# Optimization experiments

Measured on AMD Instinct MI355X. Metric: run time of the kernel, lower is better.

The kernel has to match this reference:

```python
import jax, jax.numpy as jnp
import numpy as np

EMB = 512
HEADS = 8


def setup_inputs() -> dict:
    key = jax.random.key(0)
    ks = jax.random.split(key, 5)
    B, N, E = 4, 2048, EMB
    x = jax.random.normal(ks[0], (B, N, E), dtype=jnp.float32)
    # Linear weights stored [in, out] so y = x @ W + b (matches torch x @ W.T + b with W.T)
    W_qkv = jax.random.normal(ks[1], (E, 3 * E), dtype=jnp.float32) * (E ** -0.5)
    b_qkv = jax.random.normal(ks[2], (3 * E,), dtype=jnp.float32) * 0.02
    W_proj = jax.random.normal(ks[3], (E, E), dtype=jnp.float32) * (E ** -0.5)
    b_proj = jax.random.normal(ks[4], (E,), dtype=jnp.float32) * 0.02
    return {"x": x, "W_qkv": W_qkv, "b_qkv": b_qkv, "W_proj": W_proj, "b_proj": b_proj}


def reference(x, W_qkv, b_qkv, W_proj, b_proj):
    B, N, E = x.shape
    H = HEADS
    D = E // H
    qkv = x @ W_qkv + b_qkv                      # [B, N, 3E]
    # einops 'b n (h d qkv) -> qkv b h n d': last dim splits as (h, d, 3) -> q/k/v interleaved
    qkv = qkv.reshape(B, N, H, D, 3)
    q = jnp.transpose(qkv[..., 0], (0, 2, 1, 3))  # [B, H, N, D]
    k = jnp.transpose(qkv[..., 1], (0, 2, 1, 3))
    v = jnp.transpose(qkv[..., 2], (0, 2, 1, 3))
    scale = jnp.asarray(E, x.dtype) ** 0.5        # divides by sqrt(emb_size), as in source
    energies = jnp.einsum('bhqd,bhkd->bhqk', q, k) / scale
    attention = jax.nn.softmax(energies, axis=-1)
    out = jnp.einsum('bhqk,bhkd->bhqd', attention, v)
    out = jnp.transpose(out, (0, 2, 1, 3)).reshape(B, N, E)
    return out @ W_proj + b_proj
```

## Files before the change

kernel.cpp:

```cpp
#include <hip/hip_runtime.h>
#include <hip/hip_bf16.h>

typedef __hip_bfloat16 bf16;
typedef __attribute__((ext_vector_type(8))) short short8;
typedef __attribute__((ext_vector_type(4))) float f32x4;
typedef __attribute__((ext_vector_type(16))) float f32x16;

static constexpr float QSCALE = 1.4426950408889634f / 22.627416997969522f;

__device__ __forceinline__ void gload_lds16(const void* g, void* l) {
  __builtin_amdgcn_global_load_lds((const __attribute__((address_space(1))) unsigned*)(g),
                                   (__attribute__((address_space(3))) unsigned*)(l), 16, 0, 0);
}

__device__ __forceinline__ unsigned cvtpk(float a, float b) {
  unsigned r;
  asm("v_cvt_pk_bf16_f32 %0, %1, %2" : "=v"(r) : "v"(a), "v"(b));
  return r;
}

__global__ __launch_bounds__(256) void cvt_x_kernel(const float* __restrict__ x,
                                                    bf16* __restrict__ xb, int n8) {
  for (int i = blockIdx.x * 256 + threadIdx.x; i < n8; i += gridDim.x * 256) {
    const float4* src = (const float4*)(x) + (size_t)i * 2;
    float4 a = src[0], b = src[1];
    union { short8 v; unsigned u[4]; } o;
    o.u[0] = cvtpk(a.x, a.y);
    o.u[1] = cvtpk(a.z, a.w);
    o.u[2] = cvtpk(b.x, b.y);
    o.u[3] = cvtpk(b.z, b.w);
    *(short8*)(xb + (size_t)i * 8) = o.v;
  }
}

__global__ __launch_bounds__(256) void transpose_cvt(const float* __restrict__ W,
                                                     bf16* __restrict__ Wt,
                                                     int Nout, int permute) {
  __shared__ float tile[64][65];
  const int j0 = blockIdx.x * 64, k0 = blockIdx.y * 64;
  const int tx = threadIdx.x & 63, ty = threadIdx.x >> 6;
  for (int r = ty; r < 64; r += 4)
    tile[r][tx] = W[(size_t)(k0 + r) * Nout + j0 + tx];
  __syncthreads();
  for (int r = ty; r < 64; r += 4) {
    int j = j0 + r;
    int jp = j;
    if (permute) {
      int h = j / 192, rr = j % 192, d = rr / 3, s = rr % 3;
      jp = s * 512 + h * 64 + d;
    }
    Wt[(size_t)jp * 512 + k0 + tx] = __float2bfloat16(tile[tx][r]);
  }
}

template <int MODE>
__global__ __launch_bounds__(256) void gemm_bt(const bf16* __restrict__ A,
                                               const bf16* __restrict__ Bt,
                                               const float* __restrict__ bias,
                                               bf16* __restrict__ Qb, bf16* __restrict__ Kb,
                                               bf16* __restrict__ Vt,
                                               float* __restrict__ Cout) {
  __shared__ short Alds[128 * 32];
  __shared__ short Blds[128 * 32];
  const int t = threadIdx.x;
  const int w = t >> 6;
  const int wr = w >> 1, wc = w & 1;
  const int lr = t & 15;
  const int lq = (t >> 4) & 3;
  const int bm = blockIdx.x, bn = blockIdx.y;

  f32x4 acc[4][4];
#pragma unroll
  for (int m = 0; m < 4; ++m)
#pragma unroll
    for (int n = 0; n < 4; ++n)
#pragma unroll
      for (int j = 0; j < 4; ++j) acc[m][n][j] = 0.f;

  for (int kt = 0; kt < 16; ++kt) {
#pragma unroll
    for (int i = 0; i < 2; ++i) {
      const int c = i * 256 + t;
      gload_lds16(A + (size_t)(bm * 128 + (c >> 2)) * 512 + kt * 32 + (c & 3) * 8,
                  &Alds[(i * 256 + w * 64) * 8]);
      gload_lds16(Bt + (size_t)(bn * 128 + (c >> 2)) * 512 + kt * 32 + (c & 3) * 8,
                  &Blds[(i * 256 + w * 64) * 8]);
    }
    __syncthreads();
    short8 af[4], bfr[4];
#pragma unroll
    for (int m = 0; m < 4; ++m)
      af[m] = *(const short8*)&Alds[(wr * 64 + m * 16 + lr) * 32 + lq * 8];
#pragma unroll
    for (int n = 0; n < 4; ++n)
      bfr[n] = *(const short8*)&Blds[(wc * 64 + n * 16 + lr) * 32 + lq * 8];
#pragma unroll
    for (int m = 0; m < 4; ++m)
#pragma unroll
      for (int n = 0; n < 4; ++n)
        acc[m][n] = __builtin_amdgcn_mfma_f32_16x16x32_bf16(af[m], bfr[n], acc[m][n], 0, 0, 0);
    __syncthreads();
  }

#pragma unroll
  for (int m = 0; m < 4; ++m) {
#pragma unroll
    for (int n = 0; n < 4; ++n) {
      const int col = bn * 128 + wc * 64 + n * 16 + lr;
#pragma unroll
      for (int j = 0; j < 4; ++j) {
        const int row = bm * 128 + wr * 64 + m * 16 + lq * 4 + j;
        float v = acc[m][n][j];
        if (MODE == 0) {
          const int s = col >> 9, h = (col >> 6) & 7, d = col & 63;
          v += bias[h * 192 + d * 3 + s];
          const int hd = col & 511;
          if (s == 0)
            Qb[(size_t)row * 512 + hd] = __float2bfloat16(v * QSCALE);
          else if (s == 1)
            Kb[(size_t)row * 512 + hd] = __float2bfloat16(v);
          else
            Vt[((size_t)((row >> 11) * 8 + h) * 64 + d) * 2048 + (row & 2047)] =
                __float2bfloat16(v);
        } else {
          v += bias[col];
          Cout[(size_t)row * 512 + col] = v;
        }
      }
    }
  }
}

__global__ __launch_bounds__(128) void attn_fwd(const bf16* __restrict__ Q,
                                                const bf16* __restrict__ K,
                                                const bf16* __restrict__ Vt,
                                                bf16* __restrict__ O) {
  __shared__ short Klds[2][64 * 64];
  __shared__ short Vlds[2][64 * 64];
  const int t = threadIdx.x;
  const int w = t >> 6;
  const int l = t & 63;
  const int lo = l & 31;
  const int hi = l >> 5;
  const int bid = blockIdx.x;
  const int bh = bid & 31, qt = bid >> 5;
  const int b = bh >> 3, h = bh & 7;
  const int qgA = qt * 128 + w * 64 + lo;

  const bf16* Kb = K + (size_t)b * 2048 * 512 + h * 64;
  const bf16* Vb = Vt + (size_t)bh * 64 * 2048;

  const bf16* qptrA = Q + ((size_t)b * 2048 + qgA) * 512 + h * 64 + hi * 8;
  short8 qfA[4], qfB[4];
#pragma unroll
  for (int kk = 0; kk < 4; ++kk) {
    qfA[kk] = *(const short8*)(qptrA + kk * 16);
    qfB[kk] = *(const short8*)(qptrA + 32 * 512 + kk * 16);
  }

  f32x16 zv;
#pragma unroll
  for (int r = 0; r < 16; ++r) zv[r] = 0.f;

  f32x16 accA0, accA1, accB0, accB1;
#pragma unroll
  for (int r = 0; r < 16; ++r) { accA0[r] = 0.f; accA1[r] = 0.f; accB0[r] = 0.f; accB1[r] = 0.f; }
  float lsA = 0.f, lsB = 0.f;

#define STAGE(BUF, KV0)                                                              \
  do {                                                                               \
    _Pragma("unroll") for (int i = 0; i < 4; ++i) {                                  \
      const int c = i * 128 + t, r = c >> 3, g = (c & 7) ^ (r & 7);                  \
      gload_lds16(Kb + (size_t)((KV0) + r) * 512 + g * 8,                            \
                  &Klds[BUF][(i * 128 + w * 64) * 8]);                               \
    }                                                                                \
    _Pragma("unroll") for (int i = 0; i < 4; ++i) {                                  \
      const int c = i * 128 + t, r = c >> 3, g = (c & 7) ^ (r & 7);                  \
      gload_lds16(Vb + (size_t)r * 2048 + (KV0) + g * 8,                             \
                  &Vlds[BUF][(i * 128 + w * 64) * 8]);                               \
    }                                                                                \
  } while (0)

  STAGE(0, 0);
  __syncthreads();

#pragma unroll 2
  for (int it = 0; it < 32; ++it) {
    const int buf = it & 1;
    if (it + 1 < 32) STAGE(buf ^ 1, (it + 1) * 64);

    const char* kl = (const char*)&Klds[buf][0];
    const char* vl = (const char*)&Vlds[buf][0];

#pragma unroll
    for (int sh = 0; sh < 2; ++sh) {
      short8 kf[4];
#pragma unroll
      for (int kk = 0; kk < 4; ++kk)
        kf[kk] = *(const short8*)(kl + ((sh * 32 + lo) << 7) +
                                  ((((kk << 1) | hi) ^ (lo & 7)) << 4));

      f32x16 sA, sB;
      __builtin_amdgcn_s_setprio(1);
#pragma unroll
      for (int kk = 0; kk < 4; ++kk) {
        sA = __builtin_amdgcn_mfma_f32_32x32x16_bf16(kf[kk], qfA[kk], kk ? sA : zv, 0, 0, 0);
        sB = __builtin_amdgcn_mfma_f32_32x32x16_bf16(kf[kk], qfB[kk], kk ? sB : zv, 0, 0, 0);
      }
      __builtin_amdgcn_s_setprio(0);

      short8 vf[2][2];
#pragma unroll
      for (int dt = 0; dt < 2; ++dt)
#pragma unroll
        for (int j = 0; j < 2; ++j)
          vf[dt][j] = *(const short8*)(vl + ((dt * 32 + lo) << 7) +
                                       (((((sh * 2 + j) << 1) | hi) ^ (lo & 7)) << 4));

      float tA = 0.f, tB = 0.f;
#pragma unroll
      for (int r = 0; r < 16; ++r) { sA[r] = __builtin_amdgcn_exp2f(sA[r]); tA += sA[r]; }
#pragma unroll
      for (int r = 0; r < 16; ++r) { sB[r] = __builtin_amdgcn_exp2f(sB[r]); tB += sB[r]; }
      lsA += tA;
      lsB += tB;

      short8 pbA[2], pbB[2];
#pragma unroll
      for (int g = 0; g < 2; ++g) {
        {
          unsigned a0 = cvtpk(sA[8 * g + 0], sA[8 * g + 1]);
          unsigned a1 = cvtpk(sA[8 * g + 2], sA[8 * g + 3]);
          unsigned b0 = cvtpk(sA[8 * g + 4], sA[8 * g + 5]);
          unsigned b1 = cvtpk(sA[8 * g + 6], sA[8 * g + 7]);
          asm("v_permlane32_swap_b32 %0, %1" : "+v"(a0), "+v"(b0));
          asm("v_permlane32_swap_b32 %0, %1" : "+v"(a1), "+v"(b1));
          union { unsigned u[4]; short8 v; } pu;
          pu.u[0] = a0; pu.u[1] = a1; pu.u[2] = b0; pu.u[3] = b1;
          pbA[g] = pu.v;
        }
        {
          unsigned a0 = cvtpk(sB[8 * g + 0], sB[8 * g + 1]);
          unsigned a1 = cvtpk(sB[8 * g + 2], sB[8 * g + 3]);
          unsigned b0 = cvtpk(sB[8 * g + 4], sB[8 * g + 5]);
          unsigned b1 = cvtpk(sB[8 * g + 6], sB[8 * g + 7]);
          asm("v_permlane32_swap_b32 %0, %1" : "+v"(a0), "+v"(b0));
          asm("v_permlane32_swap_b32 %0, %1" : "+v"(a1), "+v"(b1));
          union { unsigned u[4]; short8 v; } pu;
          pu.u[0] = a0; pu.u[1] = a1; pu.u[2] = b0; pu.u[3] = b1;
          pbB[g] = pu.v;
        }
      }

      __builtin_amdgcn_s_setprio(1);
#pragma unroll
      for (int j = 0; j < 2; ++j) {
        accA0 = __builtin_amdgcn_mfma_f32_32x32x16_bf16(vf[0][j], pbA[j], accA0, 0, 0, 0);
        accA1 = __builtin_amdgcn_mfma_f32_32x32x16_bf16(vf[1][j], pbA[j], accA1, 0, 0, 0);
        accB0 = __builtin_amdgcn_mfma_f32_32x32x16_bf16(vf[0][j], pbB[j], accB0, 0, 0, 0);
        accB1 = __builtin_amdgcn_mfma_f32_32x32x16_bf16(vf[1][j], pbB[j], accB1, 0, 0, 0);
      }
      __builtin_amdgcn_s_setprio(0);
    }

    __syncthreads();
  }
#undef STAGE

  lsA += __shfl_xor(lsA, 32);
  lsB += __shfl_xor(lsB, 32);
  const float rlA = 1.0f / lsA;
  const float rlB = 1.0f / lsB;
  bf16* opA = O + ((size_t)b * 2048 + qgA) * 512 + h * 64;
  bf16* opB = opA + 32 * 512;
#pragma unroll
  for (int r = 0; r < 16; ++r) {
    const int d = (r & 3) + 8 * (r >> 2) + 4 * hi;
    opA[d] = __float2bfloat16(accA0[r] * rlA);
    opA[32 + d] = __float2bfloat16(accA1[r] * rlA);
    opB[d] = __float2bfloat16(accB0[r] * rlB);
    opB[32 + d] = __float2bfloat16(accB1[r] * rlB);
  }
}

extern "C" void kernel_launch(void* const* d_in, const int* in_sizes, int n_in,
                              void* d_out, int out_size, void* d_ws, size_t ws_size,
                              hipStream_t stream) {
  const float* x = (const float*)d_in[0];
  const float* Wqkv = (const float*)d_in[1];
  const float* bqkv = (const float*)d_in[2];
  const float* Wproj = (const float*)d_in[3];
  const float* bproj = (const float*)d_in[4];
  float* out = (float*)d_out;

  char* ws = (char*)d_ws;
  bf16* xb = (bf16*)ws;
  bf16* Wqkvt = xb + (size_t)8192 * 512;
  bf16* Wprojt = Wqkvt + (size_t)1536 * 512;
  bf16* Qb = Wprojt + (size_t)512 * 512;
  bf16* Kb = Qb + (size_t)8192 * 512;
  bf16* Vt = Kb + (size_t)8192 * 512;
  bf16* Ob = xb;

  cvt_x_kernel<<<2048, 256, 0, stream>>>(x, xb, 8192 * 512 / 8);
  transpose_cvt<<<dim3(24, 8), 256, 0, stream>>>(Wqkv, Wqkvt, 1536, 1);
  transpose_cvt<<<dim3(8, 8), 256, 0, stream>>>(Wproj, Wprojt, 512, 0);
  gemm_bt<0><<<dim3(64, 12), 256, 0, stream>>>(xb, Wqkvt, bqkv, Qb, Kb, Vt, nullptr);
  attn_fwd<<<512, 128, 0, stream>>>(Qb, Kb, Vt, Ob);
  gemm_bt<1><<<dim3(64, 4), 256, 0, stream>>>(Ob, Wprojt, bproj, nullptr, nullptr, nullptr, out);
}
```

Baseline: 106.9 us.

## Split KV range across wave pairs in attention and merge partials via LDS

Doubles attention block size to four waves, with each wave pair processing half of the key/value sequence for the same query rows. Both halves are staged into doubled LDS buffers, and the loop runs half as many iterations. At the end, one half writes its accumulators and row sums to LDS and the other adds them before normalizing and storing. This raises wave-level parallelism and shortens per-wave serial loop length, at the cost of doubled LDS footprint and an extra merge step with a barrier.

Measured after the change: 111.4 us. +4.3%, slower.

```diff
diff --git a/kernel.cpp b/kernel.cpp
--- a/kernel.cpp
+++ b/kernel.cpp
@@ -131,24 +131,27 @@
   }
 }
 
-__global__ __launch_bounds__(128) void attn_fwd(const bf16* __restrict__ Q,
+__global__ __launch_bounds__(256) void attn_fwd(const bf16* __restrict__ Q,
                                                 const bf16* __restrict__ K,
                                                 const bf16* __restrict__ Vt,
                                                 bf16* __restrict__ O) {
-  __shared__ short Klds[2][64 * 64];
-  __shared__ short Vlds[2][64 * 64];
+  __shared__ short Klds[2][2][64 * 64];
+  __shared__ short Vlds[2][2][64 * 64];
   const int t = threadIdx.x;
   const int w = t >> 6;
+  const int half = w & 1;
+  const int pair = w >> 1;
   const int l = t & 63;
   const int lo = l & 31;
   const int hi = l >> 5;
   const int bid = blockIdx.x;
   const int bh = bid & 31, qt = bid >> 5;
   const int b = bh >> 3, h = bh & 7;
-  const int qgA = qt * 128 + w * 64 + lo;
+  const int qgA = qt * 128 + pair * 64 + lo;
 
   const bf16* Kb = K + (size_t)b * 2048 * 512 + h * 64;
   const bf16* Vb = Vt + (size_t)bh * 64 * 2048;
+  const int kb0 = half * 1024;
 
   const bf16* qptrA = Q + ((size_t)b * 2048 + qgA) * 512 + h * 64 + hi * 8;
   short8 qfA[4], qfB[4];
@@ -167,30 +170,32 @@
   for (int r = 0; r < 16; ++r) { accA0[r] = 0.f; accA1[r] = 0.f; accB0[r] = 0.f; accB1[r] = 0.f; }
   float lsA = 0.f, lsB = 0.f;
 
-#define STAGE(BUF, KV0)                                                              \
-  do {                                                                               \
-    _Pragma("unroll") for (int i = 0; i < 4; ++i) {                                  \
-      const int c = i * 128 + t, r = c >> 3, g = (c & 7) ^ (r & 7);                  \
-      gload_lds16(Kb + (size_t)((KV0) + r) * 512 + g * 8,                            \
-                  &Klds[BUF][(i * 128 + w * 64) * 8]);                               \
-    }                                                                                \
-    _Pragma("unroll") for (int i = 0; i < 4; ++i) {                                  \
-      const int c = i * 128 + t, r = c >> 3, g = (c & 7) ^ (r & 7);                  \
-      gload_lds16(Vb + (size_t)r * 2048 + (KV0) + g * 8,                             \
-                  &Vlds[BUF][(i * 128 + w * 64) * 8]);                               \
-    }                                                                                \
+#define STAGE(BUF, KV0)                                                               \
+  do {                                                                                \
+    _Pragma("unroll") for (int hf = 0; hf < 2; ++hf) {                                \
+      _Pragma("unroll") for (int i = 0; i < 2; ++i) {                                 \
+        const int c = i * 256 + t, r = c >> 3, g = (c & 7) ^ (r & 7);                 \
+        gload_lds16(Kb + (size_t)(hf * 1024 + (KV0) + r) * 512 + g * 8,               \
+                    &Klds[BUF][hf][(i * 256 + w * 64) * 8]);                          \
+      }                                                                               \
+      _Pragma("unroll") for (int i = 0; i < 2; ++i) {                                 \
+        const int c = i * 256 + t, r = c >> 3, g = (c & 7) ^ (r & 7);                 \
+        gload_lds16(Vb + (size_t)r * 2048 + hf * 1024 + (KV0) + g * 8,                \
+                    &Vlds[BUF][hf][(i * 256 + w * 64) * 8]);                          \
+      }                                                                               \
+    }                                                                                 \
   } while (0)
 
   STAGE(0, 0);
   __syncthreads();
 
 #pragma unroll 2
-  for (int it = 0; it < 32; ++it) {
+  for (int it = 0; it < 16; ++it) {
     const int buf = it & 1;
-    if (it + 1 < 32) STAGE(buf ^ 1, (it + 1) * 64);
-
-    const char* kl = (const char*)&Klds[buf][0];
-    const char* vl = (const char*)&Vlds[buf][0];
+    if (it + 1 < 16) STAGE(buf ^ 1, (it + 1) * 64);
+
+    const char* kl = (const char*)&Klds[buf][half][0];
+    const char* vl = (const char*)&Vlds[buf][half][0];
 
 #pragma unroll
     for (int sh = 0; sh < 2; ++sh) {
@@ -269,17 +274,45 @@
 
   lsA += __shfl_xor(lsA, 32);
   lsB += __shfl_xor(lsB, 32);
-  const float rlA = 1.0f / lsA;
-  const float rlB = 1.0f / lsB;
-  bf16* opA = O + ((size_t)b * 2048 + qgA) * 512 + h * 64;
-  bf16* opB = opA + 32 * 512;
-#pragma unroll
-  for (int r = 0; r < 16; ++r) {
-    const int d = (r & 3) + 8 * (r >> 2) + 4 * hi;
-    opA[d] = __float2bfloat16(accA0[r] * rlA);
-    opA[32 + d] = __float2bfloat16(accA1[r] * rlA);
-    opB[d] = __float2bfloat16(accB0[r] * rlB);
-    opB[32 + d] = __float2bfloat16(accB1[r] * rlB);
+
+  float* mrg = (float*)&Klds[0][0][0];
+  float* dnm = (float*)&Vlds[0][0][0];
+  if (half) {
+    float* base = mrg + pair * 4096;
+#pragma unroll
+    for (int r = 0; r < 16; ++r) {
+      base[l * 64 + ((r + l) & 63)] = accA0[r];
+      base[l * 64 + ((16 + r + l) & 63)] = accA1[r];
+      base[l * 64 + ((32 + r + l) & 63)] = accB0[r];
+      base[l * 64 + ((48 + r + l) & 63)] = accB1[r];
+    }
+    dnm[pair * 128 + l * 2] = lsA;
+    dnm[pair * 128 + l * 2 + 1] = lsB;
+  }
+  __syncthreads();
+  if (!half) {
+    float* base = mrg + pair * 4096;
+#pragma unroll
+    for (int r = 0; r < 16; ++r) {
+      accA0[r] += base[l * 64 + ((r + l) & 63)];
+      accA1[r] += base[l * 64 + ((16 + r + l) & 63)];
+      accB0[r] += base[l * 64 + ((32 + r + l) & 63)];
+      accB1[r] += base[l * 64 + ((48 + r + l) & 63)];
+    }
+    lsA += dnm[pair * 128 + l * 2];
+    lsB += dnm[pair * 128 + l * 2 + 1];
+    const float rlA = 1.0f / lsA;
+    const float rlB = 1.0f / lsB;
+    bf16* opA = O + ((size_t)b * 2048 + qgA) * 512 + h * 64;
+    bf16* opB = opA + 32 * 512;
+#pragma unroll
+    for (int r = 0; r < 16; ++r) {
+      const int d = (r & 3) + 8 * (r >> 2) + 4 * hi;
+      opA[d] = __float2bfloat16(accA0[r] * rlA);
+      opA[32 + d] = __float2bfloat16(accA1[r] * rlA);
+      opB[d] = __float2bfloat16(accB0[r] * rlB);
+      opB[32 + d] = __float2bfloat16(accB1[r] * rlB);
+    }
   }
 }
 
@@ -306,6 +339,6 @@
   transpose_cvt<<<dim3(24, 8), 256, 0, stream>>>(Wqkv, Wqkvt, 1536, 1);
   transpose_cvt<<<dim3(8, 8), 256, 0, stream>>>(Wproj, Wprojt, 512, 0);
   gemm_bt<0><<<dim3(64, 12), 256, 0, stream>>>(xb, Wqkvt, bqkv, Qb, Kb, Vt, nullptr);
-  attn_fwd<<<512, 128, 0, stream>>>(Qb, Kb, Vt, Ob);
+  attn_fwd<<<512, 256, 0, stream>>>(Qb, Kb, Vt, Ob);
   gemm_bt<1><<<dim3(64, 4), 256, 0, stream>>>(Ob, Wprojt, bproj, nullptr, nullptr, nullptr, out);
 }
```

## Compute softmax row sums via MFMA with ones and issue both QK halves upfront

Applied to the files above, without the earlier changes.

Restructures the attention inner loop so both 32-key halves of QK^T are computed before the exp/PV stages, which lets MFMA work overlap the exp and pack VALU work. Row sums are now accumulated with extra MFMAs against a ones vector instead of VALU adds and a cross-lane shuffle. Launch bounds now request at least one block per CU, which lets the compiler allocate more registers. The cost is 50% more PV-stage MFMAs, higher register pressure from the extra f32x16 accumulators, and row sums built from bf16-rounded probabilities.

After: 106.1 us. About the same (-0.7%).

```diff
diff --git a/kernel.cpp b/kernel.cpp
--- a/kernel.cpp
+++ b/kernel.cpp
@@ -17,6 +17,21 @@
   unsigned r;
   asm("v_cvt_pk_bf16_f32 %0, %1, %2" : "=v"(r) : "v"(a), "v"(b));
   return r;
+}
+
+__device__ __forceinline__ void packP(const f32x16& s, short8* pb) {
+#pragma unroll
+  for (int g = 0; g < 2; ++g) {
+    unsigned a0 = cvtpk(s[8 * g + 0], s[8 * g + 1]);
+    unsigned a1 = cvtpk(s[8 * g + 2], s[8 * g + 3]);
+    unsigned b0 = cvtpk(s[8 * g + 4], s[8 * g + 5]);
+    unsigned b1 = cvtpk(s[8 * g + 6], s[8 * g + 7]);
+    asm("v_permlane32_swap_b32 %0, %1" : "+v"(a0), "+v"(b0));
+    asm("v_permlane32_swap_b32 %0, %1" : "+v"(a1), "+v"(b1));
+    union { unsigned u[4]; short8 v; } pu;
+    pu.u[0] = a0; pu.u[1] = a1; pu.u[2] = b0; pu.u[3] = b1;
+    pb[g] = pu.v;
+  }
 }
 
 __global__ __launch_bounds__(256) void cvt_x_kernel(const float* __restrict__ x,
@@ -131,10 +146,10 @@
   }
 }
 
-__global__ __launch_bounds__(128) void attn_fwd(const bf16* __restrict__ Q,
-                                                const bf16* __restrict__ K,
-                                                const bf16* __restrict__ Vt,
-                                                bf16* __restrict__ O) {
+__global__ __launch_bounds__(128, 1) void attn_fwd(const bf16* __restrict__ Q,
+                                                   const bf16* __restrict__ K,
+                                                   const bf16* __restrict__ Vt,
+                                                   bf16* __restrict__ O) {
   __shared__ short Klds[2][64 * 64];
   __shared__ short Vlds[2][64 * 64];
   const int t = threadIdx.x;
@@ -158,14 +173,21 @@
     qfB[kk] = *(const short8*)(qptrA + 32 * 512 + kk * 16);
   }
 
+  union { unsigned u[4]; short8 v; } ones;
+#pragma unroll
+  for (int j = 0; j < 4; ++j) ones.u[j] = 0x3F803F80u;
+
   f32x16 zv;
 #pragma unroll
   for (int r = 0; r < 16; ++r) zv[r] = 0.f;
 
   f32x16 accA0, accA1, accB0, accB1;
-#pragma unroll
-  for (int r = 0; r < 16; ++r) { accA0[r] = 0.f; accA1[r] = 0.f; accB0[r] = 0.f; accB1[r] = 0.f; }
-  float lsA = 0.f, lsB = 0.f;
+  f32x16 ssumA, ssumB;
+#pragma unroll
+  for (int r = 0; r < 16; ++r) {
+    accA0[r] = 0.f; accA1[r] = 0.f; accB0[r] = 0.f; accB1[r] = 0.f;
+    ssumA[r] = 0.f; ssumB[r] = 0.f;
+  }
 
 #define STAGE(BUF, KV0)                                                              \
   do {                                                                               \
@@ -192,85 +214,89 @@
     const char* kl = (const char*)&Klds[buf][0];
     const char* vl = (const char*)&Vlds[buf][0];
 
-#pragma unroll
-    for (int sh = 0; sh < 2; ++sh) {
-      short8 kf[4];
-#pragma unroll
-      for (int kk = 0; kk < 4; ++kk)
-        kf[kk] = *(const short8*)(kl + ((sh * 32 + lo) << 7) +
-                                  ((((kk << 1) | hi) ^ (lo & 7)) << 4));
-
-      f32x16 sA, sB;
-      __builtin_amdgcn_s_setprio(1);
-#pragma unroll
-      for (int kk = 0; kk < 4; ++kk) {
-        sA = __builtin_amdgcn_mfma_f32_32x32x16_bf16(kf[kk], qfA[kk], kk ? sA : zv, 0, 0, 0);
-        sB = __builtin_amdgcn_mfma_f32_32x32x16_bf16(kf[kk], qfB[kk], kk ? sB : zv, 0, 0, 0);
-      }
-      __builtin_amdgcn_s_setprio(0);
-
-      short8 vf[2][2];
-#pragma unroll
-      for (int dt = 0; dt < 2; ++dt)
-#pragma unroll
-        for (int j = 0; j < 2; ++j)
-          vf[dt][j] = *(const short8*)(vl + ((dt * 32 + lo) << 7) +
-                                       (((((sh * 2 + j) << 1) | hi) ^ (lo & 7)) << 4));
-
-      float tA = 0.f, tB = 0.f;
-#pragma unroll
-      for (int r = 0; r < 16; ++r) { sA[r] = __builtin_amdgcn_exp2f(sA[r]); tA += sA[r]; }
-#pragma unroll
-      for (int r = 0; r < 16; ++r) { sB[r] = __builtin_amdgcn_exp2f(sB[r]); tB += sB[r]; }
-      lsA += tA;
-      lsB += tB;
-
-      short8 pbA[2], pbB[2];
-#pragma unroll
-      for (int g = 0; g < 2; ++g) {
-        {
-          unsigned a0 = cvtpk(sA[8 * g + 0], sA[8 * g + 1]);
-          unsigned a1 = cvtpk(sA[8 * g + 2], sA[8 * g + 3]);
-          unsigned b0 = cvtpk(sA[8 * g + 4], sA[8 * g + 5]);
-          unsigned b1 = cvtpk(sA[8 * g + 6], sA[8 * g + 7]);
-          asm("v_permlane32_swap_b32 %0, %1" : "+v"(a0), "+v"(b0));
-          asm("v_permlane32_swap_b32 %0, %1" : "+v"(a1), "+v"(b1));
-          union { unsigned u[4]; short8 v; } pu;
-          pu.u[0] = a0; pu.u[1] = a1; pu.u[2] = b0; pu.u[3] = b1;
-          pbA[g] = pu.v;
-        }
-        {
-          unsigned a0 = cvtpk(sB[8 * g + 0], sB[8 * g + 1]);
-          unsigned a1 = cvtpk(sB[8 * g + 2], sB[8 * g + 3]);
-          unsigned b0 = cvtpk(sB[8 * g + 4], sB[8 * g + 5]);
-          unsigned b1 = cvtpk(sB[8 * g + 6], sB[8 * g + 7]);
-          asm("v_permlane32_swap_b32 %0, %1" : "+v"(a0), "+v"(b0));
-          asm("v_permlane32_swap_b32 %0, %1" : "+v"(a1), "+v"(b1));
-          union { unsigned u[4]; short8 v; } pu;
-          pu.u[0] = a0; pu.u[1] = a1; pu.u[2] = b0; pu.u[3] = b1;
-          pbB[g] = pu.v;
-        }
-      }
-
-      __builtin_amdgcn_s_setprio(1);
-#pragma unroll
-      for (int j = 0; j < 2; ++j) {
-        accA0 = __builtin_amdgcn_mfma_f32_32x32x16_bf16(vf[0][j], pbA[j], accA0, 0, 0, 0);
-        accA1 = __builtin_amdgcn_mfma_f32_32x32x16_bf16(vf[1][j], pbA[j], accA1, 0, 0, 0);
-        accB0 = __builtin_amdgcn_mfma_f32_32x32x16_bf16(vf[0][j], pbB[j], accB0, 0, 0, 0);
-        accB1 = __builtin_amdgcn_mfma_f32_32x32x16_bf16(vf[1][j], pbB[j], accB1, 0, 0, 0);
-      }
-      __builtin_amdgcn_s_setprio(0);
-    }
+    short8 kf0[4], kf1[4];
+#pragma unroll
+    for (int kk = 0; kk < 4; ++kk) {
+      kf0[kk] = *(const short8*)(kl + (lo << 7) + ((((kk << 1) | hi) ^ (lo & 7)) << 4));
+      kf1[kk] = *(const short8*)(kl + ((32 + lo) << 7) + ((((kk << 1) | hi) ^ (lo & 7)) << 4));
+    }
+
+    f32x16 sA0, sB0, sA1, sB1;
+    __builtin_amdgcn_s_setprio(1);
+#pragma unroll
+    for (int kk = 0; kk < 4; ++kk) {
+      sA0 = __builtin_amdgcn_mfma_f32_32x32x16_bf16(kf0[kk], qfA[kk], kk ? sA0 : zv, 0, 0, 0);
+      sB0 = __builtin_amdgcn_mfma_f32_32x32x16_bf16(kf0[kk], qfB[kk], kk ? sB0 : zv, 0, 0, 0);
+    }
+#pragma unroll
+    for (int kk = 0; kk < 4; ++kk) {
+      sA1 = __builtin_amdgcn_mfma_f32_32x32x16_bf16(kf1[kk], qfA[kk], kk ? sA1 : zv, 0, 0, 0);
+      sB1 = __builtin_amdgcn_mfma_f32_32x32x16_bf16(kf1[kk], qfB[kk], kk ? sB1 : zv, 0, 0, 0);
+    }
+    __builtin_amdgcn_s_setprio(0);
+
+    short8 vf0[2][2];
+#pragma unroll
+    for (int dt = 0; dt < 2; ++dt)
+#pragma unroll
+      for (int j = 0; j < 2; ++j)
+        vf0[dt][j] = *(const short8*)(vl + ((dt * 32 + lo) << 7) +
+                                      ((((j << 1) | hi) ^ (lo & 7)) << 4));
+
+#pragma unroll
+    for (int r = 0; r < 16; ++r) sA0[r] = __builtin_amdgcn_exp2f(sA0[r]);
+#pragma unroll
+    for (int r = 0; r < 16; ++r) sB0[r] = __builtin_amdgcn_exp2f(sB0[r]);
+    short8 pbA0[2], pbB0[2];
+    packP(sA0, pbA0);
+    packP(sB0, pbB0);
+
+    __builtin_amdgcn_s_setprio(1);
+#pragma unroll
+    for (int j = 0; j < 2; ++j) {
+      accA0 = __builtin_amdgcn_mfma_f32_32x32x16_bf16(vf0[0][j], pbA0[j], accA0, 0, 0, 0);
+      accA1 = __builtin_amdgcn_mfma_f32_32x32x16_bf16(vf0[1][j], pbA0[j], accA1, 0, 0, 0);
+      accB0 = __builtin_amdgcn_mfma_f32_32x32x16_bf16(vf0[0][j], pbB0[j], accB0, 0, 0, 0);
+      accB1 = __builtin_amdgcn_mfma_f32_32x32x16_bf16(vf0[1][j], pbB0[j], accB1, 0, 0, 0);
+      ssumA = __builtin_amdgcn_mfma_f32_32x32x16_bf16(ones.v, pbA0[j], ssumA, 0, 0, 0);
+      ssumB = __builtin_amdgcn_mfma_f32_32x32x16_bf16(ones.v, pbB0[j], ssumB, 0, 0, 0);
+    }
+    __builtin_amdgcn_s_setprio(0);
+
+    short8 vf1[2][2];
+#pragma unroll
+    for (int dt = 0; dt < 2; ++dt)
+#pragma unroll
+      for (int j = 0; j < 2; ++j)
+        vf1[dt][j] = *(const short8*)(vl + ((dt * 32 + lo) << 7) +
+                                      (((((2 + j) << 1) | hi) ^ (lo & 7)) << 4));
+
+#pragma unroll
+    for (int r = 0; r < 16; ++r) sA1[r] = __builtin_amdgcn_exp2f(sA1[r]);
+#pragma unroll
+    for (int r = 0; r < 16; ++r) sB1[r] = __builtin_amdgcn_exp2f(sB1[r]);
+    short8 pbA1[2], pbB1[2];
+    packP(sA1, pbA1);
+    packP(sB1, pbB1);
+
+    __builtin_amdgcn_s_setprio(1);
+#pragma unroll
+    for (int j = 0; j < 2; ++j) {
+      accA0 = __builtin_amdgcn_mfma_f32_32x32x16_bf16(vf1[0][j], pbA1[j], accA0, 0, 0, 0);
+      accA1 = __builtin_amdgcn_mfma_f32_32x32x16_bf16(vf1[1][j], pbA1[j], accA1, 0, 0, 0);
+      accB0 = __builtin_amdgcn_mfma_f32_32x32x16_bf16(vf1[0][j], pbB1[j], accB0, 0, 0, 0);
+      accB1 = __builtin_amdgcn_mfma_f32_32x32x16_bf16(vf1[1][j], pbB1[j], accB1, 0, 0, 0);
+      ssumA = __builtin_amdgcn_mfma_f32_32x32x16_bf16(ones.v, pbA1[j], ssumA, 0, 0, 0);
+      ssumB = __builtin_amdgcn_mfma_f32_32x32x16_bf16(ones.v, pbB1[j], ssumB, 0, 0, 0);
+    }
+    __builtin_amdgcn_s_setprio(0);
 
     __syncthreads();
   }
 #undef STAGE
 
-  lsA += __shfl_xor(lsA, 32);
-  lsB += __shfl_xor(lsB, 32);
-  const float rlA = 1.0f / lsA;
-  const float rlB = 1.0f / lsB;
+  const float rlA = 1.0f / ssumA[0];
+  const float rlB = 1.0f / ssumB[0];
   bf16* opA = O + ((size_t)b * 2048 + qgA) * 512 + h * 64;
   bf16* opB = opA + 32 * 512;
 #pragma unroll
```

## Split attention KV tile across four waves and compute row sums via MFMA

Applied to the files above, without the earlier changes.

The attention kernel now launches 256 threads per block. Waves are split into two query halves and two KV halves, so each wave processes one 32-key half of each 64-key tile instead of both. The partial output accumulators and denominators are reduced through LDS at the end. Row sums of P are computed with an extra MFMA against a ones vector instead of scalar adds. This raises wave-level parallelism per CU and shortens each wave's serial loop, at the cost of extra MFMAs, an LDS reduction and a final barrier.

Result: faster. 103.6 us (-3.1%).

```diff
diff --git a/kernel.cpp b/kernel.cpp
--- a/kernel.cpp
+++ b/kernel.cpp
@@ -17,6 +17,21 @@
   unsigned r;
   asm("v_cvt_pk_bf16_f32 %0, %1, %2" : "=v"(r) : "v"(a), "v"(b));
   return r;
+}
+
+__device__ __forceinline__ void packP(const f32x16& s, short8* pb) {
+#pragma unroll
+  for (int g = 0; g < 2; ++g) {
+    unsigned a0 = cvtpk(s[8 * g + 0], s[8 * g + 1]);
+    unsigned a1 = cvtpk(s[8 * g + 2], s[8 * g + 3]);
+    unsigned b0 = cvtpk(s[8 * g + 4], s[8 * g + 5]);
+    unsigned b1 = cvtpk(s[8 * g + 6], s[8 * g + 7]);
+    asm("v_permlane32_swap_b32 %0, %1" : "+v"(a0), "+v"(b0));
+    asm("v_permlane32_swap_b32 %0, %1" : "+v"(a1), "+v"(b1));
+    union { unsigned u[4]; short8 v; } pu;
+    pu.u[0] = a0; pu.u[1] = a1; pu.u[2] = b0; pu.u[3] = b1;
+    pb[g] = pu.v;
+  }
 }
 
 __global__ __launch_bounds__(256) void cvt_x_kernel(const float* __restrict__ x,
@@ -131,21 +146,24 @@
   }
 }
 
-__global__ __launch_bounds__(128) void attn_fwd(const bf16* __restrict__ Q,
-                                                const bf16* __restrict__ K,
-                                                const bf16* __restrict__ Vt,
-                                                bf16* __restrict__ O) {
+__global__ __launch_bounds__(256, 2) void attn_fwd(const bf16* __restrict__ Q,
+                                                   const bf16* __restrict__ K,
+                                                   const bf16* __restrict__ Vt,
+                                                   bf16* __restrict__ O) {
   __shared__ short Klds[2][64 * 64];
   __shared__ short Vlds[2][64 * 64];
+  __shared__ float dnm[2][128];
   const int t = threadIdx.x;
   const int w = t >> 6;
+  const int qw = w & 1;
+  const int kh = w >> 1;
   const int l = t & 63;
   const int lo = l & 31;
   const int hi = l >> 5;
   const int bid = blockIdx.x;
   const int bh = bid & 31, qt = bid >> 5;
   const int b = bh >> 3, h = bh & 7;
-  const int qgA = qt * 128 + w * 64 + lo;
+  const int qgA = qt * 128 + qw * 64 + lo;
 
   const bf16* Kb = K + (size_t)b * 2048 * 512 + h * 64;
   const bf16* Vb = Vt + (size_t)bh * 64 * 2048;
@@ -158,26 +176,33 @@
     qfB[kk] = *(const short8*)(qptrA + 32 * 512 + kk * 16);
   }
 
+  union { unsigned u[4]; short8 v; } ones;
+#pragma unroll
+  for (int j = 0; j < 4; ++j) ones.u[j] = 0x3F803F80u;
+
   f32x16 zv;
 #pragma unroll
   for (int r = 0; r < 16; ++r) zv[r] = 0.f;
 
   f32x16 accA0, accA1, accB0, accB1;
-#pragma unroll
-  for (int r = 0; r < 16; ++r) { accA0[r] = 0.f; accA1[r] = 0.f; accB0[r] = 0.f; accB1[r] = 0.f; }
-  float lsA = 0.f, lsB = 0.f;
+  f32x16 ssumA, ssumB;
+#pragma unroll
+  for (int r = 0; r < 16; ++r) {
+    accA0[r] = 0.f; accA1[r] = 0.f; accB0[r] = 0.f; accB1[r] = 0.f;
+    ssumA[r] = 0.f; ssumB[r] = 0.f;
+  }
 
 #define STAGE(BUF, KV0)                                                              \
   do {                                                                               \
-    _Pragma("unroll") for (int i = 0; i < 4; ++i) {                                  \
-      const int c = i * 128 + t, r = c >> 3, g = (c & 7) ^ (r & 7);                  \
+    _Pragma("unroll") for (int i = 0; i < 2; ++i) {                                  \
+      const int c = i * 256 + t, r = c >> 3, g = (c & 7) ^ (r & 7);                  \
       gload_lds16(Kb + (size_t)((KV0) + r) * 512 + g * 8,                            \
-                  &Klds[BUF][(i * 128 + w * 64) * 8]);                               \
+                  &Klds[BUF][(i * 256 + w * 64) * 8]);                               \
     }                                                                                \
-    _Pragma("unroll") for (int i = 0; i < 4; ++i) {                                  \
-      const int c = i * 128 + t, r = c >> 3, g = (c & 7) ^ (r & 7);                  \
+    _Pragma("unroll") for (int i = 0; i < 2; ++i) {                                  \
+      const int c = i * 256 + t, r = c >> 3, g = (c & 7) ^ (r & 7);                  \
       gload_lds16(Vb + (size_t)r * 2048 + (KV0) + g * 8,                             \
-                  &Vlds[BUF][(i * 128 + w * 64) * 8]);                               \
+                  &Vlds[BUF][(i * 256 + w * 64) * 8]);                               \
     }                                                                                \
   } while (0)
 
@@ -192,94 +217,89 @@
     const char* kl = (const char*)&Klds[buf][0];
     const char* vl = (const char*)&Vlds[buf][0];
 
-#pragma unroll
-    for (int sh = 0; sh < 2; ++sh) {
-      short8 kf[4];
-#pragma unroll
-      for (int kk = 0; kk < 4; ++kk)
-        kf[kk] = *(const short8*)(kl + ((sh * 32 + lo) << 7) +
-                                  ((((kk << 1) | hi) ^ (lo & 7)) << 4));
-
-      f32x16 sA, sB;
-      __builtin_amdgcn_s_setprio(1);
-#pragma unroll
-      for (int kk = 0; kk < 4; ++kk) {
-        sA = __builtin_amdgcn_mfma_f32_32x32x16_bf16(kf[kk], qfA[kk], kk ? sA : zv, 0, 0, 0);
-        sB = __builtin_amdgcn_mfma_f32_32x32x16_bf16(kf[kk], qfB[kk], kk ? sB : zv, 0, 0, 0);
-      }
-      __builtin_amdgcn_s_setprio(0);
-
-      short8 vf[2][2];
-#pragma unroll
-      for (int dt = 0; dt < 2; ++dt)
-#pragma unroll
-        for (int j = 0; j < 2; ++j)
-          vf[dt][j] = *(const short8*)(vl + ((dt * 32 + lo) << 7) +
-                                       (((((sh * 2 + j) << 1) | hi) ^ (lo & 7)) << 4));
-
-      float tA = 0.f, tB = 0.f;
-#pragma unroll
-      for (int r = 0; r < 16; ++r) { sA[r] = __builtin_amdgcn_exp2f(sA[r]); tA += sA[r]; }
-#pragma unroll
-      for (int r = 0; r < 16; ++r) { sB[r] = __builtin_amdgcn_exp2f(sB[r]); tB += sB[r]; }
-      lsA += tA;
-      lsB += tB;
-
-      short8 pbA[2], pbB[2];
-#pragma unroll
-      for (int g = 0; g < 2; ++g) {
-        {
-          unsigned a0 = cvtpk(sA[8 * g + 0], sA[8 * g + 1]);
-          unsigned a1 = cvtpk(sA[8 * g + 2], sA[8 * g + 3]);
-          unsigned b0 = cvtpk(sA[8 * g + 4], sA[8 * g + 5]);
-          unsigned b1 = cvtpk(sA[8 * g + 6], sA[8 * g + 7]);
-          asm("v_permlane32_swap_b32 %0, %1" : "+v"(a0), "+v"(b0));
-          asm("v_permlane32_swap_b32 %0, %1" : "+v"(a1), "+v"(b1));
-          union { unsigned u[4]; short8 v; } pu;
-          pu.u[0] = a0; pu.u[1] = a1; pu.u[2] = b0; pu.u[3] = b1;
-          pbA[g] = pu.v;
-        }
-        {
-          unsigned a0 = cvtpk(sB[8 * g + 0], sB[8 * g + 1]);
-          unsigned a1 = cvtpk(sB[8 * g + 2], sB[8 * g + 3]);
-          unsigned b0 = cvtpk(sB[8 * g + 4], sB[8 * g + 5]);
-          unsigned b1 = cvtpk(sB[8 * g + 6], sB[8 * g + 7]);
-          asm("v_permlane32_swap_b32 %0, %1" : "+v"(a0), "+v"(b0));
-          asm("v_permlane32_swap_b32 %0, %1" : "+v"(a1), "+v"(b1));
-          union { unsigned u[4]; short8 v; } pu;
-          pu.u[0] = a0; pu.u[1] = a1; pu.u[2] = b0; pu.u[3] = b1;
-          pbB[g] = pu.v;
-        }
-      }
-
-      __builtin_amdgcn_s_setprio(1);
-#pragma unroll
-      for (int j = 0; j < 2; ++j) {
-        accA0 = __builtin_amdgcn_mfma_f32_32x32x16_bf16(vf[0][j], pbA[j], accA0, 0, 0, 0);
-        accA1 = __builtin_amdgcn_mfma_f32_32x32x16_bf16(vf[1][j], pbA[j], accA1, 0, 0, 0);
-        accB0 = __builtin_amdgcn_mfma_f32_32x32x16_bf16(vf[0][j], pbB[j], accB0, 0, 0, 0);
-        accB1 = __builtin_amdgcn_mfma_f32_32x32x16_bf16(vf[1][j], pbB[j], accB1, 0, 0, 0);
-      }
-      __builtin_amdgcn_s_setprio(0);
-    }
+    short8 kf[4];
+#pragma unroll
+    for (int kk = 0; kk < 4; ++kk)
+      kf[kk] = *(const short8*)(kl + ((kh * 32 + lo) << 7) +
+                                ((((kk << 1) | hi) ^ (lo & 7)) << 4));
+
+    f32x16 sA, sB;
+    __builtin_amdgcn_s_setprio(1);
+#pragma unroll
+    for (int kk = 0; kk < 4; ++kk) {
+      sA = __builtin_amdgcn_mfma_f32_32x32x16_bf16(kf[kk], qfA[kk], kk ? sA : zv, 0, 0, 0);
+      sB = __builtin_amdgcn_mfma_f32_32x32x16_bf16(kf[kk], qfB[kk], kk ? sB : zv, 0, 0, 0);
+    }
+    __builtin_amdgcn_s_setprio(0);
+
+    short8 vf[2][2];
+#pragma unroll
+    for (int dt = 0; dt < 2; ++dt)
+#pragma unroll
+      for (int j = 0; j < 2; ++j)
+        vf[dt][j] = *(const short8*)(vl + ((dt * 32 + lo) << 7) +
+                                     (((((kh * 2 + j) << 1) | hi) ^ (lo & 7)) << 4));
+
+#pragma unroll
+    for (int r = 0; r < 16; ++r) sA[r] = __builtin_amdgcn_exp2f(sA[r]);
+#pragma unroll
+    for (int r = 0; r < 16; ++r) sB[r] = __builtin_amdgcn_exp2f(sB[r]);
+    short8 pbA[2], pbB[2];
+    packP(sA, pbA);
+    packP(sB, pbB);
+
+    __builtin_amdgcn_s_setprio(1);
+#pragma unroll
+    for (int j = 0; j < 2; ++j) {
+      accA0 = __builtin_amdgcn_mfma_f32_32x32x16_bf16(vf[0][j], pbA[j], accA0, 0, 0, 0);
+      accA1 = __builtin_amdgcn_mfma_f32_32x32x16_bf16(vf[1][j], pbA[j], accA1, 0, 0, 0);
+      accB0 = __builtin_amdgcn_mfma_f32_32x32x16_bf16(vf[0][j], pbB[j], accB0, 0, 0, 0);
+      accB1 = __builtin_amdgcn_mfma_f32_32x32x16_bf16(vf[1][j], pbB[j], accB1, 0, 0, 0);
+      ssumA = __builtin_amdgcn_mfma_f32_32x32x16_bf16(ones.v, pbA[j], ssumA, 0, 0, 0);
+      ssumB = __builtin_amdgcn_mfma_f32_32x32x16_bf16(ones.v, pbB[j], ssumB, 0, 0, 0);
+    }
+    __builtin_amdgcn_s_setprio(0);
 
     __syncthreads();
   }
 #undef STAGE
 
-  lsA += __shfl_xor(lsA, 32);
-  lsB += __shfl_xor(lsB, 32);
-  const float rlA = 1.0f / lsA;
-  const float rlB = 1.0f / lsB;
-  bf16* opA = O + ((size_t)b * 2048 + qgA) * 512 + h * 64;
-  bf16* opB = opA + 32 * 512;
-#pragma unroll
-  for (int r = 0; r < 16; ++r) {
-    const int d = (r & 3) + 8 * (r >> 2) + 4 * hi;
-    opA[d] = __float2bfloat16(accA0[r] * rlA);
-    opA[32 + d] = __float2bfloat16(accA1[r] * rlA);
-    opB[d] = __float2bfloat16(accB0[r] * rlB);
-    opB[32 + d] = __float2bfloat16(accB1[r] * rlB);
+  float lsA = ssumA[0], lsB = ssumB[0];
+  float* base = qw ? (float*)&Vlds[0][0] : (float*)&Klds[0][0];
+  if (kh) {
+#pragma unroll
+    for (int r = 0; r < 16; ++r) {
+      base[l * 64 + ((r + l) & 63)] = accA0[r];
+      base[l * 64 + ((16 + r + l) & 63)] = accA1[r];
+      base[l * 64 + ((32 + r + l) & 63)] = accB0[r];
+      base[l * 64 + ((48 + r + l) & 63)] = accB1[r];
+    }
+    dnm[qw][l] = lsA;
+    dnm[qw][64 + l] = lsB;
+  }
+  __syncthreads();
+  if (!kh) {
+#pragma unroll
+    for (int r = 0; r < 16; ++r) {
+      accA0[r] += base[l * 64 + ((r + l) & 63)];
+      accA1[r] += base[l * 64 + ((16 + r + l) & 63)];
+      accB0[r] += base[l * 64 + ((32 + r + l) & 63)];
+      accB1[r] += base[l * 64 + ((48 + r + l) & 63)];
+    }
+    lsA += dnm[qw][l];
+    lsB += dnm[qw][64 + l];
+    const float rlA = 1.0f / lsA;
+    const float rlB = 1.0f / lsB;
+    bf16* opA = O + ((size_t)b * 2048 + qgA) * 512 + h * 64;
+    bf16* opB = opA + 32 * 512;
+#pragma unroll
+    for (int r = 0; r < 16; ++r) {
+      const int d = (r & 3) + 8 * (r >> 2) + 4 * hi;
+      opA[d] = __float2bfloat16(accA0[r] * rlA);
+      opA[32 + d] = __float2bfloat16(accA1[r] * rlA);
+      opB[d] = __float2bfloat16(accB0[r] * rlB);
+      opB[32 + d] = __float2bfloat16(accB1[r] * rlB);
+    }
   }
 }
 
@@ -306,6 +326,6 @@
   transpose_cvt<<<dim3(24, 8), 256, 0, stream>>>(Wqkv, Wqkvt, 1536, 1);
   transpose_cvt<<<dim3(8, 8), 256, 0, stream>>>(Wproj, Wprojt, 512, 0);
   gemm_bt<0><<<dim3(64, 12), 256, 0, stream>>>(xb, Wqkvt, bqkv, Qb, Kb, Vt, nullptr);
-  attn_fwd<<<512, 128, 0, stream>>>(Qb, Kb, Vt, Ob);
+  attn_fwd<<<512, 256, 0, stream>>>(Qb, Kb, Vt, Ob);
   gemm_bt<1><<<dim3(64, 4), 256, 0, stream>>>(Ob, Wprojt, bproj, nullptr, nullptr, nullptr, out);
 }
```
